# Optimization experiments

Measured on AMD Instinct MI355X. Metric: run time of the kernel, lower is better.

## Reference

```python
import jax, jax.numpy as jnp
import numpy as np

D_MODEL = 1024
NUM_HEADS = 16
HEAD_DIM = D_MODEL // NUM_HEADS
THETA = 10000.0
B, S = 2, 2048


def setup_inputs() -> dict:
    key = jax.random.key(0)
    ks = jax.random.split(key, 9)
    std = 1.0 / np.sqrt(D_MODEL)
    x = jax.random.normal(ks[0], (B, S, D_MODEL), dtype=jnp.float32)
    Wq = jax.random.normal(ks[1], (D_MODEL, D_MODEL), dtype=jnp.float32) * std
    Wk = jax.random.normal(ks[2], (D_MODEL, D_MODEL), dtype=jnp.float32) * std
    Wv = jax.random.normal(ks[3], (D_MODEL, D_MODEL), dtype=jnp.float32) * std
    Wo = jax.random.normal(ks[4], (D_MODEL, D_MODEL), dtype=jnp.float32) * std
    bq = jax.random.normal(ks[5], (D_MODEL,), dtype=jnp.float32) * std
    bk = jax.random.normal(ks[6], (D_MODEL,), dtype=jnp.float32) * std
    bv = jax.random.normal(ks[7], (D_MODEL,), dtype=jnp.float32) * std
    bo = jax.random.normal(ks[8], (D_MODEL,), dtype=jnp.float32) * std
    return {"x": x, "Wq": Wq, "bq": bq, "Wk": Wk, "bk": bk,
            "Wv": Wv, "bv": bv, "Wo": Wo, "bo": bo}


def _apply_rope(t, cos, sin):
    # t: [B, H, S, hd]; cos/sin: [S, hd//2]; interleaved-pair rotation
    t1 = t[..., 0::2]
    t2 = t[..., 1::2]
    r1 = t1 * cos - t2 * sin
    r2 = t1 * sin + t2 * cos
    return jnp.stack([r1, r2], axis=-1).reshape(t.shape)


def reference(x, Wq, bq, Wk, bk, Wv, bv, Wo, bo):
    B_, S_, D = x.shape
    H, hd = NUM_HEADS, HEAD_DIM
    # QKV projections (nn.Linear: x @ W.T + b)
    q = (x @ Wq.T + bq).reshape(B_, S_, H, hd).transpose(0, 2, 1, 3)  # [B,H,S,hd]
    k = (x @ Wk.T + bk).reshape(B_, S_, H, hd).transpose(0, 2, 1, 3)
    v = (x @ Wv.T + bv).reshape(B_, S_, H, hd).transpose(0, 2, 1, 3)
    # RoPE with token_positions = arange(S)
    pos = jnp.arange(S_, dtype=jnp.float32)
    inv_freq = 1.0 / (THETA ** (jnp.arange(0, hd, 2, dtype=jnp.float32) / hd))
    ang = pos[:, None] * inv_freq[None, :]  # [S, hd//2]
    cos, sin = jnp.cos(ang), jnp.sin(ang)
    q = _apply_rope(q, cos, sin)
    k = _apply_rope(k, cos, sin)
    # causal scaled-dot-product attention
    scores = jnp.einsum('bhqd,bhkd->bhqk', q, k) / jnp.sqrt(jnp.asarray(hd, x.dtype))
    causal = jnp.arange(S_)[:, None] >= jnp.arange(S_)[None, :]  # [S,S]
    scores = jnp.where(causal, scores, -jnp.inf)
    attn = jax.nn.softmax(scores, axis=-1)
    out = jnp.einsum('bhqk,bhkd->bhqd', attn, v)  # [B,H,S,hd]
    out = out.transpose(0, 2, 1, 3).reshape(B_, S_, D)
    return out @ Wo.T + bo
```

## Files before the change

kernel.cpp:

```cpp
#include <hip/hip_runtime.h>
#include <hip/hip_bf16.h>
#include <stdint.h>

typedef __bf16 bf16_t;
typedef __bf16 bf16x4 __attribute__((ext_vector_type(4)));
typedef __bf16 bf16x8 __attribute__((ext_vector_type(8)));
typedef float  f32x4  __attribute__((ext_vector_type(4)));

#define DM    1024
#define NH    16
#define HD    64
#define SEQ   2048
#define BATCH 2
#define BS    (BATCH*SEQ)
#define NQKV  (3*DM)

#define GLOAD_LDS16(g, l) \
  __builtin_amdgcn_global_load_lds((const __attribute__((address_space(1))) void*)(g), \
                                   (__attribute__((address_space(3))) void*)(l), 16, 0, 0)

__device__ __forceinline__ f32x4 mfma16(bf16x8 a, bf16x8 b, f32x4 c) {
  return __builtin_amdgcn_mfma_f32_16x16x32_bf16(a, b, c, 0, 0, 0);
}

__global__ __launch_bounds__(256) void k_cast_all(
    const float* __restrict__ x,  const float* __restrict__ Wq,
    const float* __restrict__ Wk, const float* __restrict__ Wv,
    const float* __restrict__ Wo, const float* __restrict__ bq,
    const float* __restrict__ bk, const float* __restrict__ bv,
    bf16_t* __restrict__ xb, bf16_t* __restrict__ Wcat,
    bf16_t* __restrict__ Wob, float* __restrict__ bcat,
    float2* __restrict__ rt)
{
  const int bid = blockIdx.x, tid = threadIdx.x;
  if (bid >= 4099) {
    const int idx = (bid - 4099) * 256 + tid;
    const int s = idx >> 5, i = idx & 31;
    float inv = powf(10000.0f, -(float)(2 * i) / 64.0f);
    float ang = (float)s * inv;
    rt[idx] = make_float2(cosf(ang), sinf(ang));
    return;
  }
  if (bid >= 4096) {
    const int k = bid - 4096;
    const float* src = (k == 0) ? bq : (k == 1) ? bk : bv;
    *(float4*)&bcat[k * DM + tid * 4] = *(const float4*)&src[tid * 4];
    return;
  }
  const float* src; bf16_t* dst; int i;
  if (bid < 2048)      { src = x;  dst = xb;                i = bid * 2048 + tid * 8; }
  else if (bid < 2560) { src = Wq; dst = Wcat;              i = (bid - 2048) * 2048 + tid * 8; }
  else if (bid < 3072) { src = Wk; dst = Wcat + DM * DM;    i = (bid - 2560) * 2048 + tid * 8; }
  else if (bid < 3584) { src = Wv; dst = Wcat + 2 * DM * DM;i = (bid - 3072) * 2048 + tid * 8; }
  else                 { src = Wo; dst = Wob;               i = (bid - 3584) * 2048 + tid * 8; }
  float4 a = *(const float4*)(src + i);
  float4 b = *(const float4*)(src + i + 4);
  bf16x8 o;
  o[0] = (bf16_t)a.x; o[1] = (bf16_t)a.y; o[2] = (bf16_t)a.z; o[3] = (bf16_t)a.w;
  o[4] = (bf16_t)b.x; o[5] = (bf16_t)b.y; o[6] = (bf16_t)b.z; o[7] = (bf16_t)b.w;
  *(bf16x8*)(dst + i) = o;
}

__global__ __launch_bounds__(256) void k_gemm_qk(
    const bf16_t* __restrict__ A, const bf16_t* __restrict__ B,
    const float* __restrict__ bias, const float2* __restrict__ rt,
    bf16_t* __restrict__ Qo, bf16_t* __restrict__ Ko)
{
  const int K = DM;
  __shared__ __align__(16) bf16_t As[2][128 * 32];
  __shared__ __align__(16) bf16_t Bs[2][128 * 32];
  const int tid  = threadIdx.x;
  const int lane = tid & 63;
  const int wave = tid >> 6;
  const int wr = wave >> 1, wc = wave & 1;
  const int m0 = blockIdx.y * 128, n0 = blockIdx.x * 128;
  const int c16 = lane & 15, g = lane >> 4;

  f32x4 acc[4][4];
  #pragma unroll
  for (int i = 0; i < 4; ++i)
    #pragma unroll
    for (int j = 0; j < 4; ++j)
      #pragma unroll
      for (int e = 0; e < 4; ++e) acc[i][j][e] = 0.0f;

  const int srow = wave * 32;
  const int lrow = lane >> 2;
  const int lk   = (lane & 3) * 8;
  const bf16_t* ga0 = A + (size_t)(m0 + srow +      lrow) * K + lk;
  const bf16_t* ga1 = A + (size_t)(m0 + srow + 16 + lrow) * K + lk;
  const bf16_t* gb0 = B + (size_t)(n0 + srow +      lrow) * K + lk;
  const bf16_t* gb1 = B + (size_t)(n0 + srow + 16 + lrow) * K + lk;
  bf16_t* la0A = &As[0][(srow) * 32];      bf16_t* la0B = &As[1][(srow) * 32];
  bf16_t* la1A = &As[0][(srow + 16) * 32]; bf16_t* la1B = &As[1][(srow + 16) * 32];
  bf16_t* lb0A = &Bs[0][(srow) * 32];      bf16_t* lb0B = &Bs[1][(srow) * 32];
  bf16_t* lb1A = &Bs[0][(srow + 16) * 32]; bf16_t* lb1B = &Bs[1][(srow + 16) * 32];

  const int po = (wr * 64 + c16) * 32 + g * 8;
  const int qo = (wc * 64 + c16) * 32 + g * 8;
  const bf16_t* paA = &As[0][po]; const bf16_t* paB = &As[1][po];
  const bf16_t* pbA = &Bs[0][qo]; const bf16_t* pbB = &Bs[1][qo];

  GLOAD_LDS16(ga0, la0A); GLOAD_LDS16(ga1, la1A);
  GLOAD_LDS16(gb0, lb0A); GLOAD_LDS16(gb1, lb1A);
  __syncthreads();

  for (int it = 0; it < K / 32; ++it) {
    const bool odd = it & 1;
    const int kt = it * 32;
    if (kt + 32 < K) {
      GLOAD_LDS16(ga0 + kt + 32, odd ? la0A : la0B);
      GLOAD_LDS16(ga1 + kt + 32, odd ? la1A : la1B);
      GLOAD_LDS16(gb0 + kt + 32, odd ? lb0A : lb0B);
      GLOAD_LDS16(gb1 + kt + 32, odd ? lb1A : lb1B);
    }
    const bf16_t* pa = odd ? paB : paA;
    const bf16_t* pb = odd ? pbB : pbA;
    bf16x8 af[4], bfr[4];
    #pragma unroll
    for (int t = 0; t < 4; ++t) af[t]  = *(const bf16x8*)(pa + t * 16 * 32);
    #pragma unroll
    for (int t = 0; t < 4; ++t) bfr[t] = *(const bf16x8*)(pb + t * 16 * 32);
    #pragma unroll
    for (int i = 0; i < 4; ++i)
      #pragma unroll
      for (int j = 0; j < 4; ++j)
        acc[i][j] = mfma16(bfr[j], af[i], acc[i][j]);
    __syncthreads();
  }

  const int region = n0 >> 10;
  bf16_t* dst = region ? Ko : Qo;
  const float qs = region ? 1.0f : (0.125f * 1.44269504088896f);
  #pragma unroll
  for (int j = 0; j < 4; ++j) {
    const int nb = n0 + wc * 64 + j * 16 + (g << 2);
    const float4 bv = *(const float4*)&bias[nb];
    const int h  = (nb >> 6) & 15;
    const int d0 = nb & 63;
    #pragma unroll
    for (int i = 0; i < 4; ++i) {
      const int m = m0 + wr * 64 + i * 16 + c16;
      const int s = m & 2047;
      const int bh = ((m >> 11) << 4) + h;
      const float4 cs = *(const float4*)&rt[(size_t)s * 32 + (d0 >> 1)];
      const float v0 = acc[i][j][0] + bv.x;
      const float v1 = acc[i][j][1] + bv.y;
      const float v2 = acc[i][j][2] + bv.z;
      const float v3 = acc[i][j][3] + bv.w;
      bf16x4 ov;
      ov[0] = (bf16_t)((v0 * cs.x - v1 * cs.y) * qs);
      ov[1] = (bf16_t)((v0 * cs.y + v1 * cs.x) * qs);
      ov[2] = (bf16_t)((v2 * cs.z - v3 * cs.w) * qs);
      ov[3] = (bf16_t)((v2 * cs.w + v3 * cs.z) * qs);
      *(bf16x4*)&dst[((size_t)bh * SEQ + s) * HD + d0] = ov;
    }
  }
}

__global__ __launch_bounds__(256) void k_gemm_v(
    const bf16_t* __restrict__ A, const bf16_t* __restrict__ B,
    const float* __restrict__ bias, bf16_t* __restrict__ Vt)
{
  const int K = DM;
  __shared__ __align__(16) bf16_t As[2][128 * 32];
  __shared__ __align__(16) bf16_t Bs[2][128 * 32];
  const int tid  = threadIdx.x;
  const int lane = tid & 63;
  const int wave = tid >> 6;
  const int wr = wave >> 1, wc = wave & 1;
  const int m0 = blockIdx.y * 128, n0 = blockIdx.x * 128;
  const int c16 = lane & 15, g = lane >> 4;

  f32x4 acc[4][4];
  #pragma unroll
  for (int i = 0; i < 4; ++i)
    #pragma unroll
    for (int j = 0; j < 4; ++j)
      #pragma unroll
      for (int e = 0; e < 4; ++e) acc[i][j][e] = 0.0f;

  const int srow = wave * 32;
  const int lrow = lane >> 2;
  const int lk   = (lane & 3) * 8;
  const bf16_t* ga0 = A + (size_t)(m0 + srow +      lrow) * K + lk;
  const bf16_t* ga1 = A + (size_t)(m0 + srow + 16 + lrow) * K + lk;
  const bf16_t* gb0 = B + (size_t)(n0 + srow +      lrow) * K + lk;
  const bf16_t* gb1 = B + (size_t)(n0 + srow + 16 + lrow) * K + lk;
  bf16_t* la0A = &As[0][(srow) * 32];      bf16_t* la0B = &As[1][(srow) * 32];
  bf16_t* la1A = &As[0][(srow + 16) * 32]; bf16_t* la1B = &As[1][(srow + 16) * 32];
  bf16_t* lb0A = &Bs[0][(srow) * 32];      bf16_t* lb0B = &Bs[1][(srow) * 32];
  bf16_t* lb1A = &Bs[0][(srow + 16) * 32]; bf16_t* lb1B = &Bs[1][(srow + 16) * 32];

  const int po = (wr * 64 + c16) * 32 + g * 8;
  const int qo = (wc * 64 + c16) * 32 + g * 8;
  const bf16_t* paA = &As[0][po]; const bf16_t* paB = &As[1][po];
  const bf16_t* pbA = &Bs[0][qo]; const bf16_t* pbB = &Bs[1][qo];

  GLOAD_LDS16(ga0, la0A); GLOAD_LDS16(ga1, la1A);
  GLOAD_LDS16(gb0, lb0A); GLOAD_LDS16(gb1, lb1A);
  __syncthreads();

  for (int it = 0; it < K / 32; ++it) {
    const bool odd = it & 1;
    const int kt = it * 32;
    if (kt + 32 < K) {
      GLOAD_LDS16(ga0 + kt + 32, odd ? la0A : la0B);
      GLOAD_LDS16(ga1 + kt + 32, odd ? la1A : la1B);
      GLOAD_LDS16(gb0 + kt + 32, odd ? lb0A : lb0B);
      GLOAD_LDS16(gb1 + kt + 32, odd ? lb1A : lb1B);
    }
    const bf16_t* pa = odd ? paB : paA;
    const bf16_t* pb = odd ? pbB : pbA;
    bf16x8 af[4], bfr[4];
    #pragma unroll
    for (int t = 0; t < 4; ++t) af[t]  = *(const bf16x8*)(pa + t * 16 * 32);
    #pragma unroll
    for (int t = 0; t < 4; ++t) bfr[t] = *(const bf16x8*)(pb + t * 16 * 32);
    #pragma unroll
    for (int i = 0; i < 4; ++i)
      #pragma unroll
      for (int j = 0; j < 4; ++j)
        acc[i][j] = mfma16(af[i], bfr[j], acc[i][j]);
    __syncthreads();
  }

  const int rbase = m0 + wr * 64 + (g << 2);
  const int cbase = n0 + wc * 64 + c16;
  #pragma unroll
  for (int j = 0; j < 4; ++j) {
    const int c = cbase + j * 16;
    const float bv = bias[c];
    const int h = (c >> 6) & 15;
    const int d = c & 63;
    #pragma unroll
    for (int i = 0; i < 4; ++i) {
      bf16x4 ov;
      #pragma unroll
      for (int e = 0; e < 4; ++e) ov[e] = (bf16_t)(acc[i][j][e] + bv);
      const int r0 = rbase + i * 16;
      const int bh = ((r0 >> 11) << 4) + h;
      const int s0 = r0 & 2047;
      const int u  = (s0 >> 4) & 3;
      const int p0 = (s0 & ~63) + ((u >> 1) << 5) + (g << 3) + ((u & 1) << 2);
      *(bf16x4*)&Vt[((size_t)bh * HD + d) * SEQ + p0] = ov;
    }
  }
}

__global__ __launch_bounds__(512) void k_gemm_out(
    const bf16_t* __restrict__ A, const bf16_t* __restrict__ B,
    const float* __restrict__ bias, float* __restrict__ C)
{
  const int K = DM, N = DM;
  __shared__ __align__(16) bf16_t As[2][128 * 32];
  __shared__ __align__(16) bf16_t Bs[2][128 * 32];
  const int tid  = threadIdx.x;
  const int lane = tid & 63;
  const int w    = tid >> 6;
  const int wr = w >> 2, wc = w & 3;
  const int m0 = blockIdx.y * 128, n0 = blockIdx.x * 128;
  const int c16 = lane & 15, g = lane >> 4;

  f32x4 acc[4][2];
  #pragma unroll
  for (int i = 0; i < 4; ++i)
    #pragma unroll
    for (int j = 0; j < 2; ++j)
      #pragma unroll
      for (int e = 0; e < 4; ++e) acc[i][j][e] = 0.0f;

  const int lrow = lane >> 2;
  const int lk   = (lane & 3) * 8;
  const bf16_t* ga = A + (size_t)(m0 + w * 16 + lrow) * K + lk;
  const bf16_t* gb = B + (size_t)(n0 + w * 16 + lrow) * K + lk;
  bf16_t* laA = &As[0][(w * 16) * 32]; bf16_t* laB = &As[1][(w * 16) * 32];
  bf16_t* lbA = &Bs[0][(w * 16) * 32]; bf16_t* lbB = &Bs[1][(w * 16) * 32];

  const int po = (wr * 64 + c16) * 32 + g * 8;
  const int qo = (wc * 32 + c16) * 32 + g * 8;
  const bf16_t* paA = &As[0][po]; const bf16_t* paB = &As[1][po];
  const bf16_t* pbA = &Bs[0][qo]; const bf16_t* pbB = &Bs[1][qo];

  GLOAD_LDS16(ga, laA); GLOAD_LDS16(gb, lbA);
  __syncthreads();

  for (int it = 0; it < K / 32; ++it) {
    const bool odd = it & 1;
    const int kt = it * 32;
    if (kt + 32 < K) {
      GLOAD_LDS16(ga + kt + 32, odd ? laA : laB);
      GLOAD_LDS16(gb + kt + 32, odd ? lbA : lbB);
    }
    const bf16_t* pa = odd ? paB : paA;
    const bf16_t* pb = odd ? pbB : pbA;
    bf16x8 af[4], bfr[2];
    #pragma unroll
    for (int t = 0; t < 4; ++t) af[t]  = *(const bf16x8*)(pa + t * 16 * 32);
    #pragma unroll
    for (int t = 0; t < 2; ++t) bfr[t] = *(const bf16x8*)(pb + t * 16 * 32);
    #pragma unroll
    for (int i = 0; i < 4; ++i)
      #pragma unroll
      for (int j = 0; j < 2; ++j)
        acc[i][j] = mfma16(af[i], bfr[j], acc[i][j]);
    __syncthreads();
  }

  const int rbase = m0 + wr * 64 + (g << 2);
  const int cbase = n0 + wc * 32 + c16;
  #pragma unroll
  for (int j = 0; j < 2; ++j) {
    const int c = cbase + j * 16;
    const float bv = bias[c];
    #pragma unroll
    for (int i = 0; i < 4; ++i) {
      #pragma unroll
      for (int e = 0; e < 4; ++e) {
        const int r = rbase + i * 16 + e;
        C[(size_t)r * N + c] = acc[i][j][e] + bv;
      }
    }
  }
}

__global__ __launch_bounds__(256, 4) void k_attn(
    const bf16_t* __restrict__ Q, const bf16_t* __restrict__ K,
    const bf16_t* __restrict__ Vt, bf16_t* __restrict__ O)
{
  __shared__ __align__(16) bf16_t kbuf[2][64 * 64];
  __shared__ __align__(16) bf16_t vbuf[2][64 * 64];
  const int tid = threadIdx.x, lane = tid & 63, w = tid >> 6;
  const int rr = blockIdx.x >> 8;
  const int kk = (blockIdx.x >> 5) & 7;
  const int bh = blockIdx.x & 31;
  const int qt = (rr == 0) ? kk : (rr == 1) ? 15 - kk : (rr == 2) ? 16 + kk : 31 - kk;
  const int b  = bh >> 4, h = bh & 15;
  const int q0 = qt * 64 + w * 16;
  const int c16 = lane & 15;
  const int g   = lane >> 4;
  const int q   = q0 + c16;

  const bf16_t* Qb = Q  + (size_t)bh * SEQ * HD;
  const bf16_t* Kb = K  + (size_t)bh * SEQ * HD;
  const bf16_t* Vb = Vt + (size_t)bh * HD * SEQ;

  bf16x8 qf0 = *(const bf16x8*)&Qb[(size_t)q * HD + g * 8];
  bf16x8 qf1 = *(const bf16x8*)&Qb[(size_t)q * HD + 32 + g * 8];

  f32x4 oacc[4];
  #pragma unroll
  for (int dblk = 0; dblk < 4; ++dblk)
    #pragma unroll
    for (int e = 0; e < 4; ++e) oacc[dblk][e] = 0.0f;
  float m_ = -1e30f, l_ = 0.0f;

  const int ntile = qt + 1;

  const int soff0 = w * 1024 + lane * 16;
  const int soff1 = soff0 + 4096;
  const int srow0 = soff0 >> 7, srow1 = soff1 >> 7;
  const int scb0  = (soff0 & 127) ^ ((srow0 & 7) << 4);
  const int scb1  = (soff1 & 127) ^ ((srow1 & 7) << 4);
  const bf16_t* gk0 = &Kb[(size_t)srow0 * HD + (scb0 >> 1)];
  const bf16_t* gk1 = &Kb[(size_t)srow1 * HD + (scb1 >> 1)];
  const bf16_t* gv0 = &Vb[(size_t)srow0 * SEQ + (scb0 >> 1)];
  const bf16_t* gv1 = &Vb[(size_t)srow1 * SEQ + (scb1 >> 1)];
  bf16_t* lk0A = &kbuf[0][(w * 1024) >> 1];
  bf16_t* lk1A = &kbuf[0][(w * 1024 + 4096) >> 1];
  bf16_t* lk0B = &kbuf[1][(w * 1024) >> 1];
  bf16_t* lk1B = &kbuf[1][(w * 1024 + 4096) >> 1];
  bf16_t* lv0A = &vbuf[0][(w * 1024) >> 1];
  bf16_t* lv1A = &vbuf[0][(w * 1024 + 4096) >> 1];
  bf16_t* lv0B = &vbuf[1][(w * 1024) >> 1];
  bf16_t* lv1B = &vbuf[1][(w * 1024 + 4096) >> 1];

  const int sw = (c16 & 7) << 4;
  const int e0 = ((16 * g) ^ sw) >> 1;
  const int dhi = (((64 + 16 * g) ^ sw) >> 1) - e0;
  const bf16_t* kp0 = &kbuf[0][c16 * 64 + e0];
  const bf16_t* kp1 = &kbuf[1][c16 * 64 + e0];
  const bf16_t* vp0 = &vbuf[0][c16 * 64 + e0];
  const bf16_t* vp1 = &vbuf[1][c16 * 64 + e0];

  GLOAD_LDS16(gk0, lk0A); GLOAD_LDS16(gk1, lk1A);
  GLOAD_LDS16(gv0, lv0A); GLOAD_LDS16(gv1, lv1A);
  gk0 += 4096; gk1 += 4096; gv0 += 64; gv1 += 64;
  __syncthreads();

  for (int t = 0; t < ntile; ++t) {
    const bool odd = t & 1;
    if (t + 1 < ntile) {
      GLOAD_LDS16(gk0, odd ? lk0A : lk0B); GLOAD_LDS16(gk1, odd ? lk1A : lk1B);
      GLOAD_LDS16(gv0, odd ? lv0A : lv0B); GLOAD_LDS16(gv1, odd ? lv1A : lv1B);
      gk0 += 4096; gk1 += 4096; gv0 += 64; gv1 += 64;
    }

    const bf16_t* kp = odd ? kp1 : kp0;
    const bf16_t* vp = odd ? vp1 : vp0;

    f32x4 st[4];
    __builtin_amdgcn_s_setprio(1);
    #pragma unroll
    for (int u = 0; u < 4; ++u) {
      bf16x8 k0 = *(const bf16x8*)(kp + u * 1024);
      bf16x8 k1 = *(const bf16x8*)(kp + u * 1024 + dhi);
      f32x4 z; z[0] = z[1] = z[2] = z[3] = 0.0f;
      z = mfma16(k0, qf0, z);
      z = mfma16(k1, qf1, z);
      st[u] = z;
    }
    __builtin_amdgcn_s_setprio(0);

    bf16x8 vlo[4], vhi[4];
    #pragma unroll
    for (int dblk = 0; dblk < 4; ++dblk) {
      vlo[dblk] = *(const bf16x8*)(vp + dblk * 1024);
      vhi[dblk] = *(const bf16x8*)(vp + dblk * 1024 + dhi);
    }

    float pv[16];
    if (t == qt) {
      const int kv0 = t * 64;
      #pragma unroll
      for (int u = 0; u < 4; ++u)
        #pragma unroll
        for (int r = 0; r < 4; ++r) {
          const int kv = kv0 + 16 * u + 4 * g + r;
          pv[u * 4 + r] = (kv <= q) ? st[u][r] : -1e30f;
        }
    } else {
      #pragma unroll
      for (int u = 0; u < 4; ++u)
        #pragma unroll
        for (int r = 0; r < 4; ++r)
          pv[u * 4 + r] = st[u][r];
    }

    float ma = fmaxf(fmaxf(pv[0], pv[1]), fmaxf(pv[2], pv[3]));
    float mb = fmaxf(fmaxf(pv[4], pv[5]), fmaxf(pv[6], pv[7]));
    float mc = fmaxf(fmaxf(pv[8], pv[9]), fmaxf(pv[10], pv[11]));
    float md = fmaxf(fmaxf(pv[12], pv[13]), fmaxf(pv[14], pv[15]));
    const float lmx = fmaxf(fmaxf(ma, mb), fmaxf(mc, md));

    if (__any(lmx - m_ > 12.0f)) {
      float mx = fmaxf(lmx, __shfl_xor(lmx, 16));
      mx = fmaxf(mx, __shfl_xor(mx, 32));
      const float mn = fmaxf(m_, mx);
      const float alpha = exp2f(m_ - mn);
      l_ *= alpha;
      #pragma unroll
      for (int dblk = 0; dblk < 4; ++dblk)
        #pragma unroll
        for (int e = 0; e < 4; ++e) oacc[dblk][e] *= alpha;
      m_ = mn;
    }

    #pragma unroll
    for (int i = 0; i < 16; ++i) pv[i] = exp2f(pv[i] - m_);
    float s0 = (pv[0] + pv[1]) + (pv[2] + pv[3]);
    float s1 = (pv[4] + pv[5]) + (pv[6] + pv[7]);
    float s2 = (pv[8] + pv[9]) + (pv[10] + pv[11]);
    float s3 = (pv[12] + pv[13]) + (pv[14] + pv[15]);
    l_ += (s0 + s1) + (s2 + s3);

    bf16x8 pf0, pf1;
    #pragma unroll
    for (int j = 0; j < 8; ++j) {
      pf0[j] = (bf16_t)pv[j];
      pf1[j] = (bf16_t)pv[8 + j];
    }

    __builtin_amdgcn_s_setprio(1);
    #pragma unroll
    for (int dblk = 0; dblk < 4; ++dblk) {
      oacc[dblk] = mfma16(vlo[dblk], pf0, oacc[dblk]);
      oacc[dblk] = mfma16(vhi[dblk], pf1, oacc[dblk]);
    }
    __builtin_amdgcn_s_setprio(0);

    __syncthreads();
  }

  l_ += __shfl_xor(l_, 16);
  l_ += __shfl_xor(l_, 32);
  const float inv = 1.0f / l_;
  bf16_t* orow = O + ((size_t)(b * SEQ + q)) * DM + h * HD;
  #pragma unroll
  for (int dblk = 0; dblk < 4; ++dblk) {
    bf16x4 ov;
    #pragma unroll
    for (int r = 0; r < 4; ++r) ov[r] = (bf16_t)(oacc[dblk][r] * inv);
    *(bf16x4*)&orow[dblk * 16 + 4 * g] = ov;
  }
}

extern "C" void kernel_launch(void* const* d_in, const int* in_sizes, int n_in,
                              void* d_out, int out_size, void* d_ws, size_t ws_size,
                              hipStream_t stream)
{
  const float* x  = (const float*)d_in[0];
  const float* Wq = (const float*)d_in[1];
  const float* bq = (const float*)d_in[2];
  const float* Wk = (const float*)d_in[3];
  const float* bk = (const float*)d_in[4];
  const float* Wv = (const float*)d_in[5];
  const float* bv = (const float*)d_in[6];
  const float* Wo = (const float*)d_in[7];
  const float* bo = (const float*)d_in[8];
  float* out = (float*)d_out;

  char* ws = (char*)d_ws;
  size_t off = 0;
  auto alloc = [&](size_t bytes) { char* p = ws + off; off += (bytes + 255) & ~255ULL; return p; };
  bf16_t* xb   = (bf16_t*)alloc((size_t)BS * DM * 2);
  bf16_t* Wcat = (bf16_t*)alloc((size_t)NQKV * DM * 2);
  bf16_t* Wob  = (bf16_t*)alloc((size_t)DM * DM * 2);
  float*  bcat = (float*)alloc((size_t)NQKV * 4);
  float2* rt   = (float2*)alloc((size_t)SEQ * 32 * 8);
  bf16_t* Qh   = (bf16_t*)alloc((size_t)BS * DM * 2);
  bf16_t* Kh   = (bf16_t*)alloc((size_t)BS * DM * 2);
  bf16_t* Vth  = (bf16_t*)alloc((size_t)BS * DM * 2);
  bf16_t* Oh   = (bf16_t*)alloc((size_t)BS * DM * 2);
  (void)ws_size; (void)in_sizes; (void)n_in; (void)out_size;

  k_cast_all<<<4099 + 256, 256, 0, stream>>>(x, Wq, Wk, Wv, Wo, bq, bk, bv,
                                             xb, Wcat, Wob, bcat, rt);

  dim3 gqk(16, 32);
  k_gemm_qk<<<gqk, 256, 0, stream>>>(xb, Wcat, bcat, rt, Qh, Kh);
  dim3 gv(8, 32);
  k_gemm_v<<<gv, 256, 0, stream>>>(xb, Wcat + 2 * DM * DM, bcat + 2 * DM, Vth);
  k_attn<<<32 * 32, 256, 0, stream>>>(Qh, Kh, Vth, Oh);
  dim3 g2(DM / 128, BS / 128);
  k_gemm_out<<<g2, 512, 0, stream>>>(Oh, Wob, bo, out);
}
```

Baseline: 122.2 us.

## Pair complementary causal query tiles per attention block to share K/V loads

Measured after the change: 121.3 us. About the same (-0.8%).

```diff
diff --git a/kernel.cpp b/kernel.cpp
--- a/kernel.cpp
+++ b/kernel.cpp
@@ -324,38 +324,39 @@
   }
 }
 
-__global__ __launch_bounds__(256, 4) void k_attn(
+__global__ __launch_bounds__(256, 2) void k_attn(
     const bf16_t* __restrict__ Q, const bf16_t* __restrict__ K,
     const bf16_t* __restrict__ Vt, bf16_t* __restrict__ O)
 {
   __shared__ __align__(16) bf16_t kbuf[2][64 * 64];
   __shared__ __align__(16) bf16_t vbuf[2][64 * 64];
   const int tid = threadIdx.x, lane = tid & 63, w = tid >> 6;
-  const int rr = blockIdx.x >> 8;
-  const int kk = (blockIdx.x >> 5) & 7;
+  const int pr = blockIdx.x >> 5;
   const int bh = blockIdx.x & 31;
-  const int qt = (rr == 0) ? kk : (rr == 1) ? 15 - kk : (rr == 2) ? 16 + kk : 31 - kk;
   const int b  = bh >> 4, h = bh & 15;
-  const int q0 = qt * 64 + w * 16;
   const int c16 = lane & 15;
   const int g   = lane >> 4;
-  const int q   = q0 + c16;
 
   const bf16_t* Qb = Q  + (size_t)bh * SEQ * HD;
   const bf16_t* Kb = K  + (size_t)bh * SEQ * HD;
   const bf16_t* Vb = Vt + (size_t)bh * HD * SEQ;
 
-  bf16x8 qf0 = *(const bf16x8*)&Qb[(size_t)q * HD + g * 8];
-  bf16x8 qf1 = *(const bf16x8*)&Qb[(size_t)q * HD + 32 + g * 8];
-
-  f32x4 oacc[4];
+  const int qtA = pr, qtB = 31 - pr;
+  const int qA  = qtA * 64 + w * 16 + c16;
+  const int qB  = qtB * 64 + w * 16 + c16;
+  const int Tmax = qtB + 1;
+
+  bf16x8 qfA0 = *(const bf16x8*)&Qb[(size_t)qA * HD + g * 8];
+  bf16x8 qfA1 = *(const bf16x8*)&Qb[(size_t)qA * HD + 32 + g * 8];
+  bf16x8 qfB0 = *(const bf16x8*)&Qb[(size_t)qB * HD + g * 8];
+  bf16x8 qfB1 = *(const bf16x8*)&Qb[(size_t)qB * HD + 32 + g * 8];
+
+  f32x4 oaccA[4], oaccB[4];
   #pragma unroll
   for (int dblk = 0; dblk < 4; ++dblk)
     #pragma unroll
-    for (int e = 0; e < 4; ++e) oacc[dblk][e] = 0.0f;
-  float m_ = -1e30f, l_ = 0.0f;
-
-  const int ntile = qt + 1;
+    for (int e = 0; e < 4; ++e) { oaccA[dblk][e] = 0.0f; oaccB[dblk][e] = 0.0f; }
+  float mA = -1e30f, lA = 0.0f, mB = -1e30f, lB = 0.0f;
 
   const int soff0 = w * 1024 + lane * 16;
   const int soff1 = soff0 + 4096;
@@ -388,9 +389,9 @@
   gk0 += 4096; gk1 += 4096; gv0 += 64; gv1 += 64;
   __syncthreads();
 
-  for (int t = 0; t < ntile; ++t) {
+  for (int t = 0; t < Tmax; ++t) {
     const bool odd = t & 1;
-    if (t + 1 < ntile) {
+    if (t + 1 < Tmax) {
       GLOAD_LDS16(gk0, odd ? lk0A : lk0B); GLOAD_LDS16(gk1, odd ? lk1A : lk1B);
       GLOAD_LDS16(gv0, odd ? lv0A : lv0B); GLOAD_LDS16(gv1, odd ? lv1A : lv1B);
       gk0 += 4096; gk1 += 4096; gv0 += 64; gv1 += 64;
@@ -399,99 +400,191 @@
     const bf16_t* kp = odd ? kp1 : kp0;
     const bf16_t* vp = odd ? vp1 : vp0;
 
-    f32x4 st[4];
-    __builtin_amdgcn_s_setprio(1);
-    #pragma unroll
-    for (int u = 0; u < 4; ++u) {
-      bf16x8 k0 = *(const bf16x8*)(kp + u * 1024);
-      bf16x8 k1 = *(const bf16x8*)(kp + u * 1024 + dhi);
-      f32x4 z; z[0] = z[1] = z[2] = z[3] = 0.0f;
-      z = mfma16(k0, qf0, z);
-      z = mfma16(k1, qf1, z);
-      st[u] = z;
-    }
-    __builtin_amdgcn_s_setprio(0);
-
-    bf16x8 vlo[4], vhi[4];
-    #pragma unroll
-    for (int dblk = 0; dblk < 4; ++dblk) {
-      vlo[dblk] = *(const bf16x8*)(vp + dblk * 1024);
-      vhi[dblk] = *(const bf16x8*)(vp + dblk * 1024 + dhi);
-    }
-
-    float pv[16];
-    if (t == qt) {
-      const int kv0 = t * 64;
-      #pragma unroll
-      for (int u = 0; u < 4; ++u)
+    {
+      f32x4 st[4];
+      __builtin_amdgcn_s_setprio(1);
+      #pragma unroll
+      for (int u = 0; u < 4; ++u) {
+        bf16x8 k0 = *(const bf16x8*)(kp + u * 1024);
+        bf16x8 k1 = *(const bf16x8*)(kp + u * 1024 + dhi);
+        f32x4 z; z[0] = z[1] = z[2] = z[3] = 0.0f;
+        z = mfma16(k0, qfB0, z);
+        z = mfma16(k1, qfB1, z);
+        st[u] = z;
+      }
+      __builtin_amdgcn_s_setprio(0);
+
+      bf16x8 vlo[4], vhi[4];
+      #pragma unroll
+      for (int dblk = 0; dblk < 4; ++dblk) {
+        vlo[dblk] = *(const bf16x8*)(vp + dblk * 1024);
+        vhi[dblk] = *(const bf16x8*)(vp + dblk * 1024 + dhi);
+      }
+
+      float pv[16];
+      if (t == qtB) {
+        const int kv0 = t * 64;
         #pragma unroll
-        for (int r = 0; r < 4; ++r) {
-          const int kv = kv0 + 16 * u + 4 * g + r;
-          pv[u * 4 + r] = (kv <= q) ? st[u][r] : -1e30f;
-        }
-    } else {
-      #pragma unroll
-      for (int u = 0; u < 4; ++u)
+        for (int u = 0; u < 4; ++u)
+          #pragma unroll
+          for (int r = 0; r < 4; ++r) {
+            const int kv = kv0 + 16 * u + 4 * g + r;
+            pv[u * 4 + r] = (kv <= qB) ? st[u][r] : -1e30f;
+          }
+      } else {
         #pragma unroll
-        for (int r = 0; r < 4; ++r)
-          pv[u * 4 + r] = st[u][r];
-    }
-
-    float ma = fmaxf(fmaxf(pv[0], pv[1]), fmaxf(pv[2], pv[3]));
-    float mb = fmaxf(fmaxf(pv[4], pv[5]), fmaxf(pv[6], pv[7]));
-    float mc = fmaxf(fmaxf(pv[8], pv[9]), fmaxf(pv[10], pv[11]));
-    float md = fmaxf(fmaxf(pv[12], pv[13]), fmaxf(pv[14], pv[15]));
-    const float lmx = fmaxf(fmaxf(ma, mb), fmaxf(mc, md));
-
-    if (__any(lmx - m_ > 12.0f)) {
-      float mx = fmaxf(lmx, __shfl_xor(lmx, 16));
-      mx = fmaxf(mx, __shfl_xor(mx, 32));
-      const float mn = fmaxf(m_, mx);
-      const float alpha = exp2f(m_ - mn);
-      l_ *= alpha;
-      #pragma unroll
-      for (int dblk = 0; dblk < 4; ++dblk)
+        for (int u = 0; u < 4; ++u)
+          #pragma unroll
+          for (int r = 0; r < 4; ++r)
+            pv[u * 4 + r] = st[u][r];
+      }
+
+      float ma = fmaxf(fmaxf(pv[0], pv[1]), fmaxf(pv[2], pv[3]));
+      float mb = fmaxf(fmaxf(pv[4], pv[5]), fmaxf(pv[6], pv[7]));
+      float mc = fmaxf(fmaxf(pv[8], pv[9]), fmaxf(pv[10], pv[11]));
+      float md = fmaxf(fmaxf(pv[12], pv[13]), fmaxf(pv[14], pv[15]));
+      const float lmx = fmaxf(fmaxf(ma, mb), fmaxf(mc, md));
+
+      if (__any(lmx - mB > 12.0f)) {
+        float mx = fmaxf(lmx, __shfl_xor(lmx, 16));
+        mx = fmaxf(mx, __shfl_xor(mx, 32));
+        const float mn = fmaxf(mB, mx);
+        const float alpha = exp2f(mB - mn);
+        lB *= alpha;
         #pragma unroll
-        for (int e = 0; e < 4; ++e) oacc[dblk][e] *= alpha;
-      m_ = mn;
-    }
-
-    #pragma unroll
-    for (int i = 0; i < 16; ++i) pv[i] = exp2f(pv[i] - m_);
-    float s0 = (pv[0] + pv[1]) + (pv[2] + pv[3]);
-    float s1 = (pv[4] + pv[5]) + (pv[6] + pv[7]);
-    float s2 = (pv[8] + pv[9]) + (pv[10] + pv[11]);
-    float s3 = (pv[12] + pv[13]) + (pv[14] + pv[15]);
-    l_ += (s0 + s1) + (s2 + s3);
-
-    bf16x8 pf0, pf1;
-    #pragma unroll
-    for (int j = 0; j < 8; ++j) {
-      pf0[j] = (bf16_t)pv[j];
-      pf1[j] = (bf16_t)pv[8 + j];
-    }
-
-    __builtin_amdgcn_s_setprio(1);
-    #pragma unroll
-    for (int dblk = 0; dblk < 4; ++dblk) {
-      oacc[dblk] = mfma16(vlo[dblk], pf0, oacc[dblk]);
-      oacc[dblk] = mfma16(vhi[dblk], pf1, oacc[dblk]);
-    }
-    __builtin_amdgcn_s_setprio(0);
+        for (int dblk = 0; dblk < 4; ++dblk)
+          #pragma unroll
+          for (int e = 0; e < 4; ++e) oaccB[dblk][e] *= alpha;
+        mB = mn;
+      }
+
+      #pragma unroll
+      for (int i = 0; i < 16; ++i) pv[i] = exp2f(pv[i] - mB);
+      float s0 = (pv[0] + pv[1]) + (pv[2] + pv[3]);
+      float s1 = (pv[4] + pv[5]) + (pv[6] + pv[7]);
+      float s2 = (pv[8] + pv[9]) + (pv[10] + pv[11]);
+      float s3 = (pv[12] + pv[13]) + (pv[14] + pv[15]);
+      lB += (s0 + s1) + (s2 + s3);
+
+      bf16x8 pf0, pf1;
+      #pragma unroll
+      for (int j = 0; j < 8; ++j) {
+        pf0[j] = (bf16_t)pv[j];
+        pf1[j] = (bf16_t)pv[8 + j];
+      }
+
+      __builtin_amdgcn_s_setprio(1);
+      #pragma unroll
+      for (int dblk = 0; dblk < 4; ++dblk) {
+        oaccB[dblk] = mfma16(vlo[dblk], pf0, oaccB[dblk]);
+        oaccB[dblk] = mfma16(vhi[dblk], pf1, oaccB[dblk]);
+      }
+      __builtin_amdgcn_s_setprio(0);
+    }
+
+    if (t <= qtA) {
+      f32x4 st[4];
+      __builtin_amdgcn_s_setprio(1);
+      #pragma unroll
+      for (int u = 0; u < 4; ++u) {
+        bf16x8 k0 = *(const bf16x8*)(kp + u * 1024);
+        bf16x8 k1 = *(const bf16x8*)(kp + u * 1024 + dhi);
+        f32x4 z; z[0] = z[1] = z[2] = z[3] = 0.0f;
+        z = mfma16(k0, qfA0, z);
+        z = mfma16(k1, qfA1, z);
+        st[u] = z;
+      }
+      __builtin_amdgcn_s_setprio(0);
+
+      bf16x8 vlo[4], vhi[4];
+      #pragma unroll
+      for (int dblk = 0; dblk < 4; ++dblk) {
+        vlo[dblk] = *(const bf16x8*)(vp + dblk * 1024);
+        vhi[dblk] = *(const bf16x8*)(vp + dblk * 1024 + dhi);
+      }
+
+      float pv[16];
+      if (t == qtA) {
+        const int kv0 = t * 64;
+        #pragma unroll
+        for (int u = 0; u < 4; ++u)
+          #pragma unroll
+          for (int r = 0; r < 4; ++r) {
+            const int kv = kv0 + 16 * u + 4 * g + r;
+            pv[u * 4 + r] = (kv <= qA) ? st[u][r] : -1e30f;
+          }
+      } else {
+        #pragma unroll
+        for (int u = 0; u < 4; ++u)
+          #pragma unroll
+          for (int r = 0; r < 4; ++r)
+            pv[u * 4 + r] = st[u][r];
+      }
+
+      float ma = fmaxf(fmaxf(pv[0], pv[1]), fmaxf(pv[2], pv[3]));
+      float mb = fmaxf(fmaxf(pv[4], pv[5]), fmaxf(pv[6], pv[7]));
+      float mc = fmaxf(fmaxf(pv[8], pv[9]), fmaxf(pv[10], pv[11]));
+      float md = fmaxf(fmaxf(pv[12], pv[13]), fmaxf(pv[14], pv[15]));
+      const float lmx = fmaxf(fmaxf(ma, mb), fmaxf(mc, md));
+
+      if (__any(lmx - mA > 12.0f)) {
+        float mx = fmaxf(lmx, __shfl_xor(lmx, 16));
+        mx = fmaxf(mx, __shfl_xor(mx, 32));
+        const float mn = fmaxf(mA, mx);
+        const float alpha = exp2f(mA - mn);
+        lA *= alpha;
+        #pragma unroll
+        for (int dblk = 0; dblk < 4; ++dblk)
+          #pragma unroll
+          for (int e = 0; e < 4; ++e) oaccA[dblk][e] *= alpha;
+        mA = mn;
+      }
+
+      #pragma unroll
+      for (int i = 0; i < 16; ++i) pv[i] = exp2f(pv[i] - mA);
+      float s0 = (pv[0] + pv[1]) + (pv[2] + pv[3]);
+      float s1 = (pv[4] + pv[5]) + (pv[6] + pv[7]);
+      float s2 = (pv[8] + pv[9]) + (pv[10] + pv[11]);
+      float s3 = (pv[12] + pv[13]) + (pv[14] + pv[15]);
+      lA += (s0 + s1) + (s2 + s3);
+
+      bf16x8 pf0, pf1;
+      #pragma unroll
+      for (int j = 0; j < 8; ++j) {
+        pf0[j] = (bf16_t)pv[j];
+        pf1[j] = (bf16_t)pv[8 + j];
+      }
+
+      __builtin_amdgcn_s_setprio(1);
+      #pragma unroll
+      for (int dblk = 0; dblk < 4; ++dblk) {
+        oaccA[dblk] = mfma16(vlo[dblk], pf0, oaccA[dblk]);
+        oaccA[dblk] = mfma16(vhi[dblk], pf1, oaccA[dblk]);
+      }
+      __builtin_amdgcn_s_setprio(0);
+    }
 
     __syncthreads();
   }
 
-  l_ += __shfl_xor(l_, 16);
-  l_ += __shfl_xor(l_, 32);
-  const float inv = 1.0f / l_;
-  bf16_t* orow = O + ((size_t)(b * SEQ + q)) * DM + h * HD;
+  lA += __shfl_xor(lA, 16);
+  lA += __shfl_xor(lA, 32);
+  lB += __shfl_xor(lB, 16);
+  lB += __shfl_xor(lB, 32);
+  const float invA = 1.0f / lA;
+  const float invB = 1.0f / lB;
+  bf16_t* orowA = O + ((size_t)(b * SEQ + qA)) * DM + h * HD;
+  bf16_t* orowB = O + ((size_t)(b * SEQ + qB)) * DM + h * HD;
   #pragma unroll
   for (int dblk = 0; dblk < 4; ++dblk) {
-    bf16x4 ov;
-    #pragma unroll
-    for (int r = 0; r < 4; ++r) ov[r] = (bf16_t)(oacc[dblk][r] * inv);
-    *(bf16x4*)&orow[dblk * 16 + 4 * g] = ov;
+    bf16x4 ovA, ovB;
+    #pragma unroll
+    for (int r = 0; r < 4; ++r) {
+      ovA[r] = (bf16_t)(oaccA[dblk][r] * invA);
+      ovB[r] = (bf16_t)(oaccB[dblk][r] * invB);
+    }
+    *(bf16x4*)&orowA[dblk * 16 + 4 * g] = ovA;
+    *(bf16x4*)&orowB[dblk * 16 + 4 * g] = ovB;
   }
 }
 
@@ -531,7 +624,7 @@
   k_gemm_qk<<<gqk, 256, 0, stream>>>(xb, Wcat, bcat, rt, Qh, Kh);
   dim3 gv(8, 32);
   k_gemm_v<<<gv, 256, 0, stream>>>(xb, Wcat + 2 * DM * DM, bcat + 2 * DM, Vth);
-  k_attn<<<32 * 32, 256, 0, stream>>>(Qh, Kh, Vth, Oh);
+  k_attn<<<512, 256, 0, stream>>>(Qh, Kh, Vth, Oh);
   dim3 g2(DM / 128, BS / 128);
   k_gemm_out<<<g2, 512, 0, stream>>>(Oh, Wob, bo, out);
 }
```

## Switch attention to 32x32x16 MFMA with 128-row query tiles per block

Applied to the files above, without the earlier changes.

New measurement: 129.1 us. +5.6%, slower.

```diff
diff --git a/kernel.cpp b/kernel.cpp
--- a/kernel.cpp
+++ b/kernel.cpp
@@ -6,6 +6,7 @@
 typedef __bf16 bf16x4 __attribute__((ext_vector_type(4)));
 typedef __bf16 bf16x8 __attribute__((ext_vector_type(8)));
 typedef float  f32x4  __attribute__((ext_vector_type(4)));
+typedef float  f32x16 __attribute__((ext_vector_type(16)));
 
 #define DM    1024
 #define NH    16
@@ -21,6 +22,9 @@
 
 __device__ __forceinline__ f32x4 mfma16(bf16x8 a, bf16x8 b, f32x4 c) {
   return __builtin_amdgcn_mfma_f32_16x16x32_bf16(a, b, c, 0, 0, 0);
+}
+__device__ __forceinline__ f32x16 mfma32(bf16x8 a, bf16x8 b, f32x16 c) {
+  return __builtin_amdgcn_mfma_f32_32x32x16_bf16(a, b, c, 0, 0, 0);
 }
 
 __global__ __launch_bounds__(256) void k_cast_all(
@@ -227,6 +231,7 @@
 
   const int rbase = m0 + wr * 64 + (g << 2);
   const int cbase = n0 + wc * 64 + c16;
+  const int gsw = ((g & 1) << 1) | (g >> 1);
   #pragma unroll
   for (int j = 0; j < 4; ++j) {
     const int c = cbase + j * 16;
@@ -241,8 +246,7 @@
       const int r0 = rbase + i * 16;
       const int bh = ((r0 >> 11) << 4) + h;
       const int s0 = r0 & 2047;
-      const int u  = (s0 >> 4) & 3;
-      const int p0 = (s0 & ~63) + ((u >> 1) << 5) + (g << 3) + ((u & 1) << 2);
+      const int p0 = (s0 & ~15) + (gsw << 2);
       *(bf16x4*)&Vt[((size_t)bh * HD + d) * SEQ + p0] = ov;
     }
   }
@@ -324,7 +328,7 @@
   }
 }
 
-__global__ __launch_bounds__(256, 4) void k_attn(
+__global__ __launch_bounds__(256, 2) void k_attn(
     const bf16_t* __restrict__ Q, const bf16_t* __restrict__ K,
     const bf16_t* __restrict__ Vt, bf16_t* __restrict__ O)
 {
@@ -334,28 +338,30 @@
   const int rr = blockIdx.x >> 8;
   const int kk = (blockIdx.x >> 5) & 7;
   const int bh = blockIdx.x & 31;
-  const int qt = (rr == 0) ? kk : (rr == 1) ? 15 - kk : (rr == 2) ? 16 + kk : 31 - kk;
+  const int qt = rr ? 15 - kk : kk;
   const int b  = bh >> 4, h = bh & 15;
-  const int q0 = qt * 64 + w * 16;
-  const int c16 = lane & 15;
-  const int g   = lane >> 4;
-  const int q   = q0 + c16;
+  const int l31 = lane & 31;
+  const int hi  = lane >> 5;
+  const int Q0  = qt * 128 + w * 32;
+  const int q   = Q0 + l31;
+  const int tD  = 2 * qt + (w >> 1);
+  const int ntb = 2 * qt + 2;
 
   const bf16_t* Qb = Q  + (size_t)bh * SEQ * HD;
   const bf16_t* Kb = K  + (size_t)bh * SEQ * HD;
   const bf16_t* Vb = Vt + (size_t)bh * HD * SEQ;
 
-  bf16x8 qf0 = *(const bf16x8*)&Qb[(size_t)q * HD + g * 8];
-  bf16x8 qf1 = *(const bf16x8*)&Qb[(size_t)q * HD + 32 + g * 8];
-
-  f32x4 oacc[4];
-  #pragma unroll
-  for (int dblk = 0; dblk < 4; ++dblk)
-    #pragma unroll
-    for (int e = 0; e < 4; ++e) oacc[dblk][e] = 0.0f;
+  bf16x8 qf[4];
+  #pragma unroll
+  for (int kc = 0; kc < 4; ++kc)
+    qf[kc] = *(const bf16x8*)&Qb[(size_t)q * HD + kc * 16 + hi * 8];
+
+  f32x16 oacc[2];
+  #pragma unroll
+  for (int dc = 0; dc < 2; ++dc)
+    #pragma unroll
+    for (int e = 0; e < 16; ++e) oacc[dc][e] = 0.0f;
   float m_ = -1e30f, l_ = 0.0f;
-
-  const int ntile = qt + 1;
 
   const int soff0 = w * 1024 + lane * 16;
   const int soff1 = soff0 + 4096;
@@ -375,124 +381,124 @@
   bf16_t* lv0B = &vbuf[1][(w * 1024) >> 1];
   bf16_t* lv1B = &vbuf[1][(w * 1024 + 4096) >> 1];
 
-  const int sw = (c16 & 7) << 4;
-  const int e0 = ((16 * g) ^ sw) >> 1;
-  const int dhi = (((64 + 16 * g) ^ sw) >> 1) - e0;
-  const bf16_t* kp0 = &kbuf[0][c16 * 64 + e0];
-  const bf16_t* kp1 = &kbuf[1][c16 * 64 + e0];
-  const bf16_t* vp0 = &vbuf[0][c16 * 64 + e0];
-  const bf16_t* vp1 = &vbuf[1][c16 * 64 + e0];
+  const int swz = (l31 & 7) << 4;
+  int eK[4];
+  #pragma unroll
+  for (int kc = 0; kc < 4; ++kc)
+    eK[kc] = ((kc * 32 + hi * 16) ^ swz) >> 1;
+  const bf16_t* kpb0 = &kbuf[0][l31 * 64];
+  const bf16_t* kpb1 = &kbuf[1][l31 * 64];
+  const bf16_t* vpb0 = &vbuf[0][l31 * 64];
+  const bf16_t* vpb1 = &vbuf[1][l31 * 64];
 
   GLOAD_LDS16(gk0, lk0A); GLOAD_LDS16(gk1, lk1A);
   GLOAD_LDS16(gv0, lv0A); GLOAD_LDS16(gv1, lv1A);
   gk0 += 4096; gk1 += 4096; gv0 += 64; gv1 += 64;
   __syncthreads();
 
-  for (int t = 0; t < ntile; ++t) {
+  for (int t = 0; t < ntb; ++t) {
     const bool odd = t & 1;
-    if (t + 1 < ntile) {
+    if (t + 1 < ntb) {
       GLOAD_LDS16(gk0, odd ? lk0A : lk0B); GLOAD_LDS16(gk1, odd ? lk1A : lk1B);
       GLOAD_LDS16(gv0, odd ? lv0A : lv0B); GLOAD_LDS16(gv1, odd ? lv1A : lv1B);
       gk0 += 4096; gk1 += 4096; gv0 += 64; gv1 += 64;
     }
 
-    const bf16_t* kp = odd ? kp1 : kp0;
-    const bf16_t* vp = odd ? vp1 : vp0;
-
-    f32x4 st[4];
-    __builtin_amdgcn_s_setprio(1);
-    #pragma unroll
-    for (int u = 0; u < 4; ++u) {
-      bf16x8 k0 = *(const bf16x8*)(kp + u * 1024);
-      bf16x8 k1 = *(const bf16x8*)(kp + u * 1024 + dhi);
-      f32x4 z; z[0] = z[1] = z[2] = z[3] = 0.0f;
-      z = mfma16(k0, qf0, z);
-      z = mfma16(k1, qf1, z);
-      st[u] = z;
-    }
-    __builtin_amdgcn_s_setprio(0);
-
-    bf16x8 vlo[4], vhi[4];
-    #pragma unroll
-    for (int dblk = 0; dblk < 4; ++dblk) {
-      vlo[dblk] = *(const bf16x8*)(vp + dblk * 1024);
-      vhi[dblk] = *(const bf16x8*)(vp + dblk * 1024 + dhi);
-    }
-
-    float pv[16];
-    if (t == qt) {
-      const int kv0 = t * 64;
-      #pragma unroll
-      for (int u = 0; u < 4; ++u)
-        #pragma unroll
-        for (int r = 0; r < 4; ++r) {
-          const int kv = kv0 + 16 * u + 4 * g + r;
-          pv[u * 4 + r] = (kv <= q) ? st[u][r] : -1e30f;
+    if (t <= tD) {
+      const bf16_t* kp = odd ? kpb1 : kpb0;
+      const bf16_t* vp = odd ? vpb1 : vpb0;
+
+      f32x16 sacc[2];
+      __builtin_amdgcn_s_setprio(1);
+      #pragma unroll
+      for (int kvc = 0; kvc < 2; ++kvc) {
+        f32x16 z;
+        #pragma unroll
+        for (int e = 0; e < 16; ++e) z[e] = 0.0f;
+        #pragma unroll
+        for (int kc = 0; kc < 4; ++kc) {
+          bf16x8 kf = *(const bf16x8*)(kp + kvc * 2048 + eK[kc]);
+          z = mfma32(kf, qf[kc], z);
         }
-    } else {
-      #pragma unroll
-      for (int u = 0; u < 4; ++u)
-        #pragma unroll
-        for (int r = 0; r < 4; ++r)
-          pv[u * 4 + r] = st[u][r];
-    }
-
-    float ma = fmaxf(fmaxf(pv[0], pv[1]), fmaxf(pv[2], pv[3]));
-    float mb = fmaxf(fmaxf(pv[4], pv[5]), fmaxf(pv[6], pv[7]));
-    float mc = fmaxf(fmaxf(pv[8], pv[9]), fmaxf(pv[10], pv[11]));
-    float md = fmaxf(fmaxf(pv[12], pv[13]), fmaxf(pv[14], pv[15]));
-    const float lmx = fmaxf(fmaxf(ma, mb), fmaxf(mc, md));
-
-    if (__any(lmx - m_ > 12.0f)) {
-      float mx = fmaxf(lmx, __shfl_xor(lmx, 16));
-      mx = fmaxf(mx, __shfl_xor(mx, 32));
-      const float mn = fmaxf(m_, mx);
-      const float alpha = exp2f(m_ - mn);
-      l_ *= alpha;
-      #pragma unroll
-      for (int dblk = 0; dblk < 4; ++dblk)
-        #pragma unroll
-        for (int e = 0; e < 4; ++e) oacc[dblk][e] *= alpha;
-      m_ = mn;
-    }
-
-    #pragma unroll
-    for (int i = 0; i < 16; ++i) pv[i] = exp2f(pv[i] - m_);
-    float s0 = (pv[0] + pv[1]) + (pv[2] + pv[3]);
-    float s1 = (pv[4] + pv[5]) + (pv[6] + pv[7]);
-    float s2 = (pv[8] + pv[9]) + (pv[10] + pv[11]);
-    float s3 = (pv[12] + pv[13]) + (pv[14] + pv[15]);
-    l_ += (s0 + s1) + (s2 + s3);
-
-    bf16x8 pf0, pf1;
-    #pragma unroll
-    for (int j = 0; j < 8; ++j) {
-      pf0[j] = (bf16_t)pv[j];
-      pf1[j] = (bf16_t)pv[8 + j];
-    }
-
-    __builtin_amdgcn_s_setprio(1);
-    #pragma unroll
-    for (int dblk = 0; dblk < 4; ++dblk) {
-      oacc[dblk] = mfma16(vlo[dblk], pf0, oacc[dblk]);
-      oacc[dblk] = mfma16(vhi[dblk], pf1, oacc[dblk]);
-    }
-    __builtin_amdgcn_s_setprio(0);
+        sacc[kvc] = z;
+      }
+      __builtin_amdgcn_s_setprio(0);
+
+      float pv[32];
+      if (t == tD) {
+        const int kv0 = t * 64;
+        #pragma unroll
+        for (int kvc = 0; kvc < 2; ++kvc)
+          #pragma unroll
+          for (int reg = 0; reg < 16; ++reg) {
+            const int kv = kv0 + kvc * 32 + (reg & 3) + 8 * (reg >> 2) + 4 * hi;
+            pv[kvc * 16 + reg] = (kv <= q) ? sacc[kvc][reg] : -1e30f;
+          }
+      } else {
+        #pragma unroll
+        for (int kvc = 0; kvc < 2; ++kvc)
+          #pragma unroll
+          for (int reg = 0; reg < 16; ++reg)
+            pv[kvc * 16 + reg] = sacc[kvc][reg];
+      }
+
+      float mx01 = fmaxf(pv[0], pv[1]);
+      #pragma unroll
+      for (int i = 2; i < 32; i += 2) mx01 = fmaxf(mx01, fmaxf(pv[i], pv[i + 1]));
+      const float lmx = mx01;
+
+      if (__any(lmx - m_ > 12.0f)) {
+        float mx = fmaxf(lmx, __shfl_xor(lmx, 32));
+        const float mn = fmaxf(m_, mx);
+        const float alpha = exp2f(m_ - mn);
+        l_ *= alpha;
+        #pragma unroll
+        for (int dc = 0; dc < 2; ++dc)
+          #pragma unroll
+          for (int e = 0; e < 16; ++e) oacc[dc][e] *= alpha;
+        m_ = mn;
+      }
+
+      #pragma unroll
+      for (int i = 0; i < 32; ++i) pv[i] = exp2f(pv[i] - m_);
+      float ps = 0.0f;
+      #pragma unroll
+      for (int i = 0; i < 32; ++i) ps += pv[i];
+      l_ += ps;
+
+      bf16x8 pf[4];
+      #pragma unroll
+      for (int f = 0; f < 4; ++f)
+        #pragma unroll
+        for (int e = 0; e < 8; ++e)
+          pf[f][e] = (bf16_t)pv[(f >> 1) * 16 + (f & 1) * 8 + e];
+
+      __builtin_amdgcn_s_setprio(1);
+      #pragma unroll
+      for (int dc = 0; dc < 2; ++dc)
+        #pragma unroll
+        for (int f = 0; f < 4; ++f) {
+          bf16x8 vf = *(const bf16x8*)(vp + dc * 2048 + eK[f]);
+          oacc[dc] = mfma32(vf, pf[f], oacc[dc]);
+        }
+      __builtin_amdgcn_s_setprio(0);
+    }
 
     __syncthreads();
   }
 
-  l_ += __shfl_xor(l_, 16);
   l_ += __shfl_xor(l_, 32);
   const float inv = 1.0f / l_;
   bf16_t* orow = O + ((size_t)(b * SEQ + q)) * DM + h * HD;
   #pragma unroll
-  for (int dblk = 0; dblk < 4; ++dblk) {
-    bf16x4 ov;
-    #pragma unroll
-    for (int r = 0; r < 4; ++r) ov[r] = (bf16_t)(oacc[dblk][r] * inv);
-    *(bf16x4*)&orow[dblk * 16 + 4 * g] = ov;
-  }
+  for (int dc = 0; dc < 2; ++dc)
+    #pragma unroll
+    for (int rb = 0; rb < 4; ++rb) {
+      bf16x4 ov;
+      #pragma unroll
+      for (int r = 0; r < 4; ++r) ov[r] = (bf16_t)(oacc[dc][rb * 4 + r] * inv);
+      *(bf16x4*)&orow[dc * 32 + rb * 8 + 4 * hi] = ov;
+    }
 }
 
 extern "C" void kernel_launch(void* const* d_in, const int* in_sizes, int n_in,
@@ -531,7 +537,7 @@
   k_gemm_qk<<<gqk, 256, 0, stream>>>(xb, Wcat, bcat, rt, Qh, Kh);
   dim3 gv(8, 32);
   k_gemm_v<<<gv, 256, 0, stream>>>(xb, Wcat + 2 * DM * DM, bcat + 2 * DM, Vth);
-  k_attn<<<32 * 32, 256, 0, stream>>>(Qh, Kh, Vth, Oh);
+  k_attn<<<512, 256, 0, stream>>>(Qh, Kh, Vth, Oh);
   dim3 g2(DM / 128, BS / 128);
   k_gemm_out<<<g2, 512, 0, stream>>>(Oh, Wob, bo, out);
 }
```
